# Optimization experiments

Hardware: AMD Instinct MI355X
Metric: run time of the kernel (lower is better)

## Reference

```python
import jax, jax.numpy as jnp
import numpy as np

B, T, C, H, D = 4, 2048, 1024, 16, 64  # batch, seq, n_embd, n_head, head_size


def setup_inputs() -> dict:
    key = jax.random.key(0)
    ks = jax.random.split(key, 8)
    s = 0.02  # init scale for weights
    return {
        "q": jax.random.normal(ks[0], (B, T, C), jnp.float32),
        "k": jax.random.normal(ks[1], (B, T, C), jnp.float32),
        "v": jax.random.normal(ks[2], (B, T, C), jnp.float32),
        "Wq": jax.random.normal(ks[3], (H, C, D), jnp.float32) * s,
        "Wk": jax.random.normal(ks[4], (H, C, D), jnp.float32) * s,
        "Wv": jax.random.normal(ks[5], (H, C, D), jnp.float32) * s,
        "Wo": jax.random.normal(ks[6], (H * D, C), jnp.float32) * s,
        "bo": jnp.zeros((C,), jnp.float32),
    }


def reference(q, k, v, Wq, Wk, Wv, Wo, bo):
    # Per-head projections (vectorized over heads): [B,T,C] x [H,C,D] -> [B,H,T,D]
    qh = jnp.einsum('btc,hcd->bhtd', q, Wq)
    kh = jnp.einsum('btc,hcd->bhtd', k, Wk)
    vh = jnp.einsum('btc,hcd->bhtd', v, Wv)
    # NOTE: source divides by sqrt(C) = sqrt(n_embd), not sqrt(head_size)
    scale = 1.0 / jnp.sqrt(jnp.float32(C))
    att = jnp.einsum('bhtd,bhsd->bhts', qh, kh) * scale  # [B,H,T,T]
    causal = jnp.tril(jnp.ones((T, T), dtype=bool))
    att = jnp.where(causal, att, -jnp.inf)
    p = jax.nn.softmax(att, axis=-1)  # dropout is identity in eval mode
    out = jnp.einsum('bhts,bhsd->bhtd', p, vh)
    # concat heads in order: [B,H,T,D] -> [B,T,H*D]
    out = out.transpose(0, 2, 1, 3).reshape(B, T, H * D)
    return out @ Wo + bo
```

## Files before the change

### kernel.cpp

```cpp
#include <hip/hip_runtime.h>
#include <hip/hip_bf16.h>
#include <cstdint>
#include <cstddef>

#define B_  4
#define T_  2048
#define C_  1024
#define H_  16
#define D_  64
#define MROWS (B_*T_)
#define NDIM  (H_*D_)

typedef float  f32x4 __attribute__((ext_vector_type(4)));
typedef __bf16 bfrag __attribute__((ext_vector_type(8)));

__device__ __forceinline__ unsigned short f2bf(float f) {
  union { float f; unsigned u; } v; v.f = f;
  unsigned r = v.u + 0x7fffu + ((v.u >> 16) & 1u);
  return (unsigned short)(r >> 16);
}

__device__ __forceinline__ void async_load16(const void* g, void* l) {
  __builtin_amdgcn_global_load_lds((__attribute__((address_space(1))) void*)(void*)g,
                                   (__attribute__((address_space(3))) void*)l,
                                   16, 0, 0);
}

__device__ __forceinline__ unsigned pack_bf2(float f0, float f1) {
  unsigned a0 = __float_as_uint(f0) + 0x8000u;
  unsigned a1 = __float_as_uint(f1) + 0x8000u;
  return __builtin_amdgcn_perm(a1, a0, 0x07060302u);
}

__global__ __launch_bounds__(256) void cvt_bf16_kernel(
    const float* __restrict__ a, const float* __restrict__ b, const float* __restrict__ c,
    unsigned short* __restrict__ oa, unsigned short* __restrict__ ob, unsigned short* __restrict__ oc,
    int n)
{
  const float* in = blockIdx.z == 0 ? a : blockIdx.z == 1 ? b : c;
  unsigned short* out = blockIdx.z == 0 ? oa : blockIdx.z == 1 ? ob : oc;
  int i = (blockIdx.x * 256 + threadIdx.x) * 4;
  if (i < n) {
    float4 v = *(const float4*)(in + i);
    ushort4 r;
    r.x = f2bf(v.x); r.y = f2bf(v.y); r.z = f2bf(v.z); r.w = f2bf(v.w);
    *(ushort4*)(out + i) = r;
  }
}

__global__ __launch_bounds__(256) void transpose_wqkv_kernel(
    const float* __restrict__ Wq, const float* __restrict__ Wk, const float* __restrict__ Wv,
    unsigned short* __restrict__ Oq, unsigned short* __restrict__ Ok, unsigned short* __restrict__ Ov)
{
  int z = blockIdx.z; int sel = z >> 4, h = z & 15;
  const float* in = (sel == 0 ? Wq : sel == 1 ? Wk : Wv) + (size_t)h * C_ * D_;
  unsigned short* out = (sel == 0 ? Oq : sel == 1 ? Ok : Ov) + (size_t)h * D_ * C_;
  __shared__ float tile[64][65];
  int c0 = blockIdx.x * 64;
  int x = threadIdx.x & 63, y4 = threadIdx.x >> 6;
  for (int r = y4; r < 64; r += 4)
    tile[r][x] = in[(size_t)(c0 + r) * D_ + x];
  __syncthreads();
  for (int r = y4; r < 64; r += 4)
    out[(size_t)r * C_ + c0 + x] = f2bf(tile[x][r]);
}

__global__ __launch_bounds__(256) void transpose_wo_kernel(
    const float* __restrict__ Wo, unsigned short* __restrict__ outT)
{
  __shared__ float tile[64][65];
  int i0 = blockIdx.x * 64, j0 = blockIdx.y * 64;
  int x = threadIdx.x & 63, y4 = threadIdx.x >> 6;
  for (int r = y4; r < 64; r += 4)
    tile[r][x] = Wo[(size_t)(i0 + r) * C_ + j0 + x];
  __syncthreads();
  for (int r = y4; r < 64; r += 4)
    outT[(size_t)(j0 + r) * NDIM + i0 + x] = f2bf(tile[x][r]);
}

template <int EPI>
__global__ __launch_bounds__(256) void gemm_bt_kernel(
    const unsigned short* __restrict__ A0, const unsigned short* __restrict__ A1, const unsigned short* __restrict__ A2,
    const unsigned short* __restrict__ B0, const unsigned short* __restrict__ B1, const unsigned short* __restrict__ B2,
    void* C0, void* C1, void* C2, const float* __restrict__ bias,
    int M, int N, int K)
{
  const unsigned short* A  = blockIdx.z == 0 ? A0 : blockIdx.z == 1 ? A1 : A2;
  const unsigned short* Bt = blockIdx.z == 0 ? B0 : blockIdx.z == 1 ? B1 : B2;
  void* Cv                 = blockIdx.z == 0 ? C0 : blockIdx.z == 1 ? C1 : C2;

  __shared__ __align__(16) short As[128 * 64];
  __shared__ __align__(16) short Bs[128 * 64];

  const int tid = threadIdx.x, lane = tid & 63, wave = tid >> 6;
  const int quad = lane >> 4, l15 = lane & 15;
  const int m0 = blockIdx.y * 128, n0 = blockIdx.x * 128;
  const int wm = (wave >> 1) * 64, wn = (wave & 1) * 64;

  f32x4 acc[4][4] = {};

  for (int k0 = 0; k0 < K; k0 += 64) {
#pragma unroll
    for (int i = 0; i < 4; ++i) {
      int p0 = (wave * 4 + i) * 64;
      int p = p0 + lane;
      int m = p >> 3, cl = (p & 7) ^ (m & 7);
      async_load16(A  + (size_t)(m0 + m) * K + k0 + cl * 8, (char*)As + p0 * 16);
      async_load16(Bt + (size_t)(n0 + m) * K + k0 + cl * 8, (char*)Bs + p0 * 16);
    }
    __syncthreads();
#pragma unroll
    for (int ks = 0; ks < 2; ++ks) {
      bfrag af[4], bf[4];
#pragma unroll
      for (int i = 0; i < 4; ++i) {
        int m = wm + i * 16 + l15;
        int c = (ks * 4 + quad) ^ (m & 7);
        af[i] = *(const bfrag*)(As + m * 64 + c * 8);
        int n = wn + i * 16 + l15;
        int c2 = (ks * 4 + quad) ^ (n & 7);
        bf[i] = *(const bfrag*)(Bs + n * 64 + c2 * 8);
      }
#pragma unroll
      for (int i = 0; i < 4; ++i)
#pragma unroll
        for (int j = 0; j < 4; ++j)
          acc[i][j] = __builtin_amdgcn_mfma_f32_16x16x32_bf16(af[i], bf[j], acc[i][j], 0, 0, 0);
    }
    __syncthreads();
  }

  if constexpr (EPI == 0) {
    unsigned short* Cb = (unsigned short*)Cv;
#pragma unroll
    for (int i = 0; i < 4; ++i) {
      int row0 = m0 + wm + i * 16 + quad * 4;
#pragma unroll
      for (int j = 0; j < 4; ++j) {
        int col = n0 + wn + j * 16 + l15;
#pragma unroll
        for (int r = 0; r < 4; ++r)
          Cb[(size_t)(row0 + r) * N + col] = f2bf(acc[i][j][r]);
      }
    }
  } else if constexpr (EPI == 1) {
    float* Cf = (float*)Cv;
#pragma unroll
    for (int j = 0; j < 4; ++j) {
      int col = n0 + wn + j * 16 + l15;
      float bv = bias[col];
#pragma unroll
      for (int i = 0; i < 4; ++i) {
        int row0 = m0 + wm + i * 16 + quad * 4;
#pragma unroll
        for (int r = 0; r < 4; ++r)
          Cf[(size_t)(row0 + r) * N + col] = acc[i][j][r] + bv;
      }
    }
  } else {
    unsigned short* Vo = (unsigned short*)Cv;
#pragma unroll
    for (int i = 0; i < 4; ++i) {
      int m = m0 + wm + i * 16 + quad * 4;
      int bb = m >> 11, tt = m & 2047;
#pragma unroll
      for (int j = 0; j < 4; ++j) {
        int n = n0 + wn + j * 16 + l15;
        int hh = n >> 6, dd = n & 63;
        ushort4 pk;
        pk.x = f2bf(acc[i][j][0]); pk.y = f2bf(acc[i][j][1]);
        pk.z = f2bf(acc[i][j][2]); pk.w = f2bf(acc[i][j][3]);
        *(ushort4*)(Vo + (((size_t)bb * 16 + hh) * 64 + dd) * T_ + tt) = pk;
      }
    }
  }
}

__global__ __launch_bounds__(256, 4) void flash_kernel(
    const unsigned short* __restrict__ Qh, const unsigned short* __restrict__ Kh,
    const unsigned short* __restrict__ VT, unsigned short* __restrict__ Oh)
{
  __shared__ __align__(16) short Ks[64 * 64];
  __shared__ __align__(16) short Vt[64 * 64];
  __shared__ __align__(16) short Ps[4][32 * 72];

  const int tid = threadIdx.x, lane = tid & 63, wave = tid >> 6;
  const int quad = lane >> 4, l15 = lane & 15;
  const int id = blockIdx.x;
  const int rr = id >> 8, cc = id & 255, g = cc >> 6, bh = cc & 63;
  const int t = (rr == 0) ? g : (rr == 1) ? 7 - g : (rr == 2) ? 8 + g : 15 - g;
  const int b = bh >> 4, h = bh & 15;
  const int q0 = t * 128;

  const unsigned short* Qbase = Qh + (size_t)b * T_ * NDIM + h * 64;
  const unsigned short* Kbase = Kh + (size_t)b * T_ * NDIM + h * 64;
  const unsigned short* Vbase = VT + ((size_t)(b * 16 + h) * 64) * T_;

  const int wrow_lo = q0 + wave * 32;

  bfrag qfr[2][2];
#pragma unroll
  for (int j = 0; j < 2; ++j)
#pragma unroll
    for (int ks = 0; ks < 2; ++ks)
      qfr[j][ks] = *(const bfrag*)(Qbase + (size_t)(wrow_lo + j * 16 + l15) * NDIM + ks * 32 + quad * 8);

  float l_st[2] = {0.f, 0.f};
  f32x4 o_acc[2][4] = {};
  short* pw = &Ps[wave][0];
  const float c32 = 0.045084220f;

  for (int kv0 = 0; kv0 <= q0 + 64; kv0 += 64) {
#pragma unroll
    for (int i = 0; i < 2; ++i) {
      int p0 = (wave * 2 + i) * 64;
      int p = p0 + lane;
      int r = p >> 3, cl = (p & 7) ^ (r & 7);
      async_load16(Kbase + (size_t)(kv0 + r) * NDIM + cl * 8, (char*)Ks + p0 * 16);
      async_load16(Vbase + (size_t)r * T_ + kv0 + cl * 8, (char*)Vt + p0 * 16);
    }
    __syncthreads();

    if (kv0 <= wrow_lo + 31) {
      f32x4 sv[2][4] = {};
#pragma unroll
      for (int ks = 0; ks < 2; ++ks) {
        bfrag kf[4];
#pragma unroll
        for (int i = 0; i < 4; ++i) {
          int key = i * 16 + l15;
          int c = (ks * 4 + quad) ^ (key & 7);
          kf[i] = *(const bfrag*)(Ks + key * 64 + c * 8);
        }
#pragma unroll
        for (int j = 0; j < 2; ++j)
#pragma unroll
          for (int i = 0; i < 4; ++i)
            sv[j][i] = __builtin_amdgcn_mfma_f32_16x16x32_bf16(kf[i], qfr[j][ks], sv[j][i], 0, 0, 0);
      }

#pragma unroll
      for (int j = 0; j < 2; ++j)
#pragma unroll
        for (int i = 0; i < 4; ++i)
#pragma unroll
          for (int r = 0; r < 4; ++r)
            sv[j][i][r] = __builtin_amdgcn_exp2f(sv[j][i][r] * c32);
      if (kv0 + 63 > wrow_lo) {
#pragma unroll
        for (int j = 0; j < 2; ++j) {
          int qr = wrow_lo + j * 16 + l15;
#pragma unroll
          for (int i = 0; i < 4; ++i) {
            int keyb = kv0 + i * 16 + quad * 4;
#pragma unroll
            for (int r = 0; r < 4; ++r)
              if (keyb + r > qr) sv[j][i][r] = 0.f;
          }
        }
      }

#pragma unroll
      for (int j = 0; j < 2; ++j) {
#pragma unroll
        for (int i = 0; i < 4; ++i) {
          l_st[j] += sv[j][i][0] + sv[j][i][1] + sv[j][i][2] + sv[j][i][3];
          uint2 pk;
          pk.x = pack_bf2(sv[j][i][0], sv[j][i][1]);
          pk.y = pack_bf2(sv[j][i][2], sv[j][i][3]);
          *(uint2*)(pw + (j * 16 + l15) * 72 + i * 16 + quad * 4) = pk;
        }
      }

#pragma unroll
      for (int ks = 0; ks < 2; ++ks) {
        bfrag vf[4], pf[2];
#pragma unroll
        for (int i2 = 0; i2 < 4; ++i2) {
          int d = i2 * 16 + l15;
          int c = (ks * 4 + quad) ^ (d & 7);
          vf[i2] = *(const bfrag*)(Vt + d * 64 + c * 8);
        }
#pragma unroll
        for (int j = 0; j < 2; ++j)
          pf[j] = *(const bfrag*)(pw + (j * 16 + l15) * 72 + ks * 32 + quad * 8);
#pragma unroll
        for (int j = 0; j < 2; ++j)
#pragma unroll
          for (int i2 = 0; i2 < 4; ++i2)
            o_acc[j][i2] = __builtin_amdgcn_mfma_f32_16x16x32_bf16(vf[i2], pf[j], o_acc[j][i2], 0, 0, 0);
      }
    }
    __syncthreads();
  }

#pragma unroll
  for (int j = 0; j < 2; ++j) {
    float s = l_st[j];
    s += __shfl_xor(s, 16, 64);
    s += __shfl_xor(s, 32, 64);
    float inv = 1.f / s;
    int qr = q0 + wave * 32 + j * 16 + l15;
    size_t base = ((size_t)b * T_ + qr) * NDIM + h * 64;
#pragma unroll
    for (int i2 = 0; i2 < 4; ++i2) {
      ushort4 pk;
      pk.x = f2bf(o_acc[j][i2][0] * inv);
      pk.y = f2bf(o_acc[j][i2][1] * inv);
      pk.z = f2bf(o_acc[j][i2][2] * inv);
      pk.w = f2bf(o_acc[j][i2][3] * inv);
      *(ushort4*)(Oh + base + i2 * 16 + quad * 4) = pk;
    }
  }
}

extern "C" void kernel_launch(void* const* d_in, const int* in_sizes, int n_in,
                              void* d_out, int out_size, void* d_ws, size_t ws_size,
                              hipStream_t stream)
{
  const float* q  = (const float*)d_in[0];
  const float* k  = (const float*)d_in[1];
  const float* v  = (const float*)d_in[2];
  const float* Wq = (const float*)d_in[3];
  const float* Wk = (const float*)d_in[4];
  const float* Wv = (const float*)d_in[5];
  const float* Wo = (const float*)d_in[6];
  const float* bo = (const float*)d_in[7];
  float* out = (float*)d_out;

  char* w = (char*)d_ws;
  const size_t szBTC = (size_t)MROWS * C_ * 2;
  const size_t szW   = (size_t)NDIM * C_ * 2;
  unsigned short* qb   = (unsigned short*)(w);
  unsigned short* kb   = (unsigned short*)(w + szBTC);
  unsigned short* vb   = (unsigned short*)(w + 2 * szBTC);
  unsigned short* wqT  = (unsigned short*)(w + 3 * szBTC);
  unsigned short* wkT  = (unsigned short*)(w + 3 * szBTC + szW);
  unsigned short* wvT  = (unsigned short*)(w + 3 * szBTC + 2 * szW);
  unsigned short* woT  = (unsigned short*)(w + 3 * szBTC + 3 * szW);
  unsigned short* qhp  = (unsigned short*)(w + 3 * szBTC + 4 * szW);
  unsigned short* khp  = (unsigned short*)(w + 4 * szBTC + 4 * szW);
  unsigned short* vT   = (unsigned short*)(w + 5 * szBTC + 4 * szW);
  unsigned short* attO = (unsigned short*)(w + 6 * szBTC + 4 * szW);

  const int nElems = MROWS * C_;

  cvt_bf16_kernel<<<dim3(nElems / 1024, 1, 3), 256, 0, stream>>>(q, k, v, qb, kb, vb, nElems);
  transpose_wqkv_kernel<<<dim3(C_ / 64, 1, 48), 256, 0, stream>>>(Wq, Wk, Wv, wqT, wkT, wvT);
  transpose_wo_kernel<<<dim3(NDIM / 64, C_ / 64, 1), 256, 0, stream>>>(Wo, woT);

  gemm_bt_kernel<0><<<dim3(NDIM / 128, MROWS / 128, 2), 256, 0, stream>>>(
      qb, kb, nullptr, wqT, wkT, nullptr, qhp, khp, nullptr, nullptr, MROWS, NDIM, C_);
  gemm_bt_kernel<2><<<dim3(NDIM / 128, MROWS / 128, 1), 256, 0, stream>>>(
      vb, nullptr, nullptr, wvT, nullptr, nullptr, vT, nullptr, nullptr, nullptr, MROWS, NDIM, C_);

  flash_kernel<<<dim3(1024), 256, 0, stream>>>(qhp, khp, vT, attO);

  gemm_bt_kernel<1><<<dim3(C_ / 128, MROWS / 128, 1), 256, 0, stream>>>(
      attO, attO, attO, woT, woT, woT, out, out, out, bo, MROWS, C_, NDIM);
}
```

Before: 346.5 us.

## Merge prep kernels, fuse QKV GEMM launches, widen flash KV tile to 128

Folds the activation conversion and both weight transposes into one prep kernel, and runs the Q/K/V projections as a single 3-slice GEMM launch with a per-slice epilogue. This removes launch overhead and tail gaps between small kernels. The flash kernel now loads 128 keys per barrier round, processed as two 64-key halves, which halves the number of syncs. The cost is more shared memory per block, so the occupancy hint drops from 4 to 3 blocks.

```diff
diff --git a/kernel.cpp b/kernel.cpp
--- a/kernel.cpp
+++ b/kernel.cpp
@@ -32,50 +32,48 @@
   return __builtin_amdgcn_perm(a1, a0, 0x07060302u);
 }
 
-__global__ __launch_bounds__(256) void cvt_bf16_kernel(
-    const float* __restrict__ a, const float* __restrict__ b, const float* __restrict__ c,
-    unsigned short* __restrict__ oa, unsigned short* __restrict__ ob, unsigned short* __restrict__ oc,
-    int n)
+__global__ __launch_bounds__(256) void prep_kernel(
+    const float* __restrict__ q, const float* __restrict__ k, const float* __restrict__ v,
+    unsigned short* __restrict__ qb, unsigned short* __restrict__ kb, unsigned short* __restrict__ vb,
+    const float* __restrict__ Wq, const float* __restrict__ Wk, const float* __restrict__ Wv,
+    unsigned short* __restrict__ wqT, unsigned short* __restrict__ wkT, unsigned short* __restrict__ wvT,
+    const float* __restrict__ Wo, unsigned short* __restrict__ woT)
 {
-  const float* in = blockIdx.z == 0 ? a : blockIdx.z == 1 ? b : c;
-  unsigned short* out = blockIdx.z == 0 ? oa : blockIdx.z == 1 ? ob : oc;
-  int i = (blockIdx.x * 256 + threadIdx.x) * 4;
-  if (i < n) {
-    float4 v = *(const float4*)(in + i);
+  const int id = blockIdx.x, tid = threadIdx.x;
+  if (id < 24576) {
+    int z = id >> 13, blk = id & 8191;
+    const float* in = z == 0 ? q : z == 1 ? k : v;
+    unsigned short* out = z == 0 ? qb : z == 1 ? kb : vb;
+    int i = (blk * 256 + tid) * 4;
+    float4 vv = *(const float4*)(in + i);
     ushort4 r;
-    r.x = f2bf(v.x); r.y = f2bf(v.y); r.z = f2bf(v.z); r.w = f2bf(v.w);
+    r.x = f2bf(vv.x); r.y = f2bf(vv.y); r.z = f2bf(vv.z); r.w = f2bf(vv.w);
     *(ushort4*)(out + i) = r;
-  }
-}
-
-__global__ __launch_bounds__(256) void transpose_wqkv_kernel(
-    const float* __restrict__ Wq, const float* __restrict__ Wk, const float* __restrict__ Wv,
-    unsigned short* __restrict__ Oq, unsigned short* __restrict__ Ok, unsigned short* __restrict__ Ov)
-{
-  int z = blockIdx.z; int sel = z >> 4, h = z & 15;
-  const float* in = (sel == 0 ? Wq : sel == 1 ? Wk : Wv) + (size_t)h * C_ * D_;
-  unsigned short* out = (sel == 0 ? Oq : sel == 1 ? Ok : Ov) + (size_t)h * D_ * C_;
-  __shared__ float tile[64][65];
-  int c0 = blockIdx.x * 64;
-  int x = threadIdx.x & 63, y4 = threadIdx.x >> 6;
-  for (int r = y4; r < 64; r += 4)
-    tile[r][x] = in[(size_t)(c0 + r) * D_ + x];
-  __syncthreads();
-  for (int r = y4; r < 64; r += 4)
-    out[(size_t)r * C_ + c0 + x] = f2bf(tile[x][r]);
-}
-
-__global__ __launch_bounds__(256) void transpose_wo_kernel(
-    const float* __restrict__ Wo, unsigned short* __restrict__ outT)
-{
-  __shared__ float tile[64][65];
-  int i0 = blockIdx.x * 64, j0 = blockIdx.y * 64;
-  int x = threadIdx.x & 63, y4 = threadIdx.x >> 6;
-  for (int r = y4; r < 64; r += 4)
-    tile[r][x] = Wo[(size_t)(i0 + r) * C_ + j0 + x];
-  __syncthreads();
-  for (int r = y4; r < 64; r += 4)
-    outT[(size_t)(j0 + r) * NDIM + i0 + x] = f2bf(tile[x][r]);
+  } else if (id < 25344) {
+    int u = id - 24576;
+    int z = u >> 4, cblk = u & 15;
+    int sel = z >> 4, h = z & 15;
+    const float* in = (sel == 0 ? Wq : sel == 1 ? Wk : Wv) + (size_t)h * C_ * D_;
+    unsigned short* out = (sel == 0 ? wqT : sel == 1 ? wkT : wvT) + (size_t)h * D_ * C_;
+    __shared__ float tile[64][65];
+    int c0 = cblk * 64;
+    int x = tid & 63, y4 = tid >> 6;
+    for (int r = y4; r < 64; r += 4)
+      tile[r][x] = in[(size_t)(c0 + r) * D_ + x];
+    __syncthreads();
+    for (int r = y4; r < 64; r += 4)
+      out[(size_t)r * C_ + c0 + x] = f2bf(tile[x][r]);
+  } else {
+    int u = id - 25344;
+    __shared__ float tile[64][65];
+    int i0 = (u >> 4) * 64, j0 = (u & 15) * 64;
+    int x = tid & 63, y4 = tid >> 6;
+    for (int r = y4; r < 64; r += 4)
+      tile[r][x] = Wo[(size_t)(i0 + r) * C_ + j0 + x];
+    __syncthreads();
+    for (int r = y4; r < 64; r += 4)
+      woT[(size_t)(j0 + r) * NDIM + i0 + x] = f2bf(tile[x][r]);
+  }
 }
 
 template <int EPI>
@@ -131,19 +129,37 @@
   }
 
   if constexpr (EPI == 0) {
-    unsigned short* Cb = (unsigned short*)Cv;
-#pragma unroll
-    for (int i = 0; i < 4; ++i) {
-      int row0 = m0 + wm + i * 16 + quad * 4;
-#pragma unroll
-      for (int j = 0; j < 4; ++j) {
-        int col = n0 + wn + j * 16 + l15;
-#pragma unroll
-        for (int r = 0; r < 4; ++r)
-          Cb[(size_t)(row0 + r) * N + col] = f2bf(acc[i][j][r]);
-      }
-    }
-  } else if constexpr (EPI == 1) {
+    if (blockIdx.z < 2) {
+      unsigned short* Cb = (unsigned short*)Cv;
+#pragma unroll
+      for (int i = 0; i < 4; ++i) {
+        int row0 = m0 + wm + i * 16 + quad * 4;
+#pragma unroll
+        for (int j = 0; j < 4; ++j) {
+          int col = n0 + wn + j * 16 + l15;
+#pragma unroll
+          for (int r = 0; r < 4; ++r)
+            Cb[(size_t)(row0 + r) * N + col] = f2bf(acc[i][j][r]);
+        }
+      }
+    } else {
+      unsigned short* Vo = (unsigned short*)Cv;
+#pragma unroll
+      for (int i = 0; i < 4; ++i) {
+        int m = m0 + wm + i * 16 + quad * 4;
+        int bb = m >> 11, tt = m & 2047;
+#pragma unroll
+        for (int j = 0; j < 4; ++j) {
+          int n = n0 + wn + j * 16 + l15;
+          int hh = n >> 6, dd = n & 63;
+          ushort4 pk;
+          pk.x = f2bf(acc[i][j][0]); pk.y = f2bf(acc[i][j][1]);
+          pk.z = f2bf(acc[i][j][2]); pk.w = f2bf(acc[i][j][3]);
+          *(ushort4*)(Vo + (((size_t)bb * 16 + hh) * 64 + dd) * T_ + tt) = pk;
+        }
+      }
+    }
+  } else {
     float* Cf = (float*)Cv;
 #pragma unroll
     for (int j = 0; j < 4; ++j) {
@@ -157,31 +173,15 @@
           Cf[(size_t)(row0 + r) * N + col] = acc[i][j][r] + bv;
       }
     }
-  } else {
-    unsigned short* Vo = (unsigned short*)Cv;
-#pragma unroll
-    for (int i = 0; i < 4; ++i) {
-      int m = m0 + wm + i * 16 + quad * 4;
-      int bb = m >> 11, tt = m & 2047;
-#pragma unroll
-      for (int j = 0; j < 4; ++j) {
-        int n = n0 + wn + j * 16 + l15;
-        int hh = n >> 6, dd = n & 63;
-        ushort4 pk;
-        pk.x = f2bf(acc[i][j][0]); pk.y = f2bf(acc[i][j][1]);
-        pk.z = f2bf(acc[i][j][2]); pk.w = f2bf(acc[i][j][3]);
-        *(ushort4*)(Vo + (((size_t)bb * 16 + hh) * 64 + dd) * T_ + tt) = pk;
-      }
-    }
-  }
-}
-
-__global__ __launch_bounds__(256, 4) void flash_kernel(
+  }
+}
+
+__global__ __launch_bounds__(256, 3) void flash_kernel(
     const unsigned short* __restrict__ Qh, const unsigned short* __restrict__ Kh,
     const unsigned short* __restrict__ VT, unsigned short* __restrict__ Oh)
 {
-  __shared__ __align__(16) short Ks[64 * 64];
-  __shared__ __align__(16) short Vt[64 * 64];
+  __shared__ __align__(16) short Ks[128 * 64];
+  __shared__ __align__(16) short Vt[2][64 * 64];
   __shared__ __align__(16) short Ps[4][32 * 72];
 
   const int tid = threadIdx.x, lane = tid & 63, wave = tid >> 6;
@@ -210,18 +210,23 @@
   short* pw = &Ps[wave][0];
   const float c32 = 0.045084220f;
 
-  for (int kv0 = 0; kv0 <= q0 + 64; kv0 += 64) {
-#pragma unroll
-    for (int i = 0; i < 2; ++i) {
-      int p0 = (wave * 2 + i) * 64;
+  for (int kv0 = 0; kv0 < q0 + 128; kv0 += 128) {
+#pragma unroll
+    for (int i = 0; i < 4; ++i) {
+      int p0 = (wave * 4 + i) * 64;
       int p = p0 + lane;
-      int r = p >> 3, cl = (p & 7) ^ (r & 7);
-      async_load16(Kbase + (size_t)(kv0 + r) * NDIM + cl * 8, (char*)Ks + p0 * 16);
-      async_load16(Vbase + (size_t)r * T_ + kv0 + cl * 8, (char*)Vt + p0 * 16);
-    }
-    __syncthreads();
-
-    if (kv0 <= wrow_lo + 31) {
+      int kr = p >> 3, kcl = (p & 7) ^ (kr & 7);
+      async_load16(Kbase + (size_t)(kv0 + kr) * NDIM + kcl * 8, (char*)Ks + p0 * 16);
+      int hh = p >> 9, d = (p >> 3) & 63, vcl = (p & 7) ^ (d & 7);
+      async_load16(Vbase + (size_t)d * T_ + kv0 + hh * 64 + vcl * 8, (char*)Vt + p0 * 16);
+    }
+    __syncthreads();
+
+#pragma unroll
+    for (int hf = 0; hf < 2; ++hf) {
+      const int kvh = kv0 + hf * 64;
+      if (kvh > wrow_lo + 31) break;
+
       f32x4 sv[2][4] = {};
 #pragma unroll
       for (int ks = 0; ks < 2; ++ks) {
@@ -230,7 +235,7 @@
         for (int i = 0; i < 4; ++i) {
           int key = i * 16 + l15;
           int c = (ks * 4 + quad) ^ (key & 7);
-          kf[i] = *(const bfrag*)(Ks + key * 64 + c * 8);
+          kf[i] = *(const bfrag*)(Ks + (hf * 64 + key) * 64 + c * 8);
         }
 #pragma unroll
         for (int j = 0; j < 2; ++j)
@@ -246,13 +251,13 @@
 #pragma unroll
           for (int r = 0; r < 4; ++r)
             sv[j][i][r] = __builtin_amdgcn_exp2f(sv[j][i][r] * c32);
-      if (kv0 + 63 > wrow_lo) {
+      if (kvh + 63 > wrow_lo) {
 #pragma unroll
         for (int j = 0; j < 2; ++j) {
           int qr = wrow_lo + j * 16 + l15;
 #pragma unroll
           for (int i = 0; i < 4; ++i) {
-            int keyb = kv0 + i * 16 + quad * 4;
+            int keyb = kvh + i * 16 + quad * 4;
 #pragma unroll
             for (int r = 0; r < 4; ++r)
               if (keyb + r > qr) sv[j][i][r] = 0.f;
@@ -279,7 +284,7 @@
         for (int i2 = 0; i2 < 4; ++i2) {
           int d = i2 * 16 + l15;
           int c = (ks * 4 + quad) ^ (d & 7);
-          vf[i2] = *(const bfrag*)(Vt + d * 64 + c * 8);
+          vf[i2] = *(const bfrag*)(&Vt[hf][0] + d * 64 + c * 8);
         }
 #pragma unroll
         for (int j = 0; j < 2; ++j)
@@ -343,16 +348,11 @@
   unsigned short* vT   = (unsigned short*)(w + 5 * szBTC + 4 * szW);
   unsigned short* attO = (unsigned short*)(w + 6 * szBTC + 4 * szW);
 
-  const int nElems = MROWS * C_;
-
-  cvt_bf16_kernel<<<dim3(nElems / 1024, 1, 3), 256, 0, stream>>>(q, k, v, qb, kb, vb, nElems);
-  transpose_wqkv_kernel<<<dim3(C_ / 64, 1, 48), 256, 0, stream>>>(Wq, Wk, Wv, wqT, wkT, wvT);
-  transpose_wo_kernel<<<dim3(NDIM / 64, C_ / 64, 1), 256, 0, stream>>>(Wo, woT);
-
-  gemm_bt_kernel<0><<<dim3(NDIM / 128, MROWS / 128, 2), 256, 0, stream>>>(
-      qb, kb, nullptr, wqT, wkT, nullptr, qhp, khp, nullptr, nullptr, MROWS, NDIM, C_);
-  gemm_bt_kernel<2><<<dim3(NDIM / 128, MROWS / 128, 1), 256, 0, stream>>>(
-      vb, nullptr, nullptr, wvT, nullptr, nullptr, vT, nullptr, nullptr, nullptr, MROWS, NDIM, C_);
+  prep_kernel<<<dim3(25600), 256, 0, stream>>>(q, k, v, qb, kb, vb,
+                                               Wq, Wk, Wv, wqT, wkT, wvT, Wo, woT);
+
+  gemm_bt_kernel<0><<<dim3(NDIM / 128, MROWS / 128, 3), 256, 0, stream>>>(
+      qb, kb, vb, wqT, wkT, wvT, qhp, khp, vT, nullptr, MROWS, NDIM, C_);
 
   flash_kernel<<<dim3(1024), 256, 0, stream>>>(qhp, khp, vT, attO);
 
```

After: 319.1 us. 7.9% less time.
